# Kernel tuning notes

Measured on AMD Instinct MI355X. Metric: run time of the kernel, lower is better.

The kernel has to match this reference:

```python
import jax, jax.numpy as jnp
from jax import lax
import numpy as np

NUM_CLASSES = 81
SCALES = (64.0, 128.0, 256.0)
RATIOS = (0.5, 1.0, 2.0)
A = 9                       # anchors per cell = len(SCALES)*len(RATIOS)
POOL = 14
PRE_NMS = 6000
PROPOSAL_COUNT = 1000
NMS_THR = 0.7
BN_EPS = 1e-3               # keras BatchNormalization default epsilon
NEG = -1e9                  # suppressed-score sentinel (avoids -inf NaNs in grad)


def conv(x, w, b, padding):
    return lax.conv_general_dilated(x, w, (1, 1), padding,
        dimension_numbers=('NHWC', 'HWIO', 'NHWC')) + b


def bn(x, g, b, m, v):
    # inference-mode batch norm
    return (x - m) * (g / jnp.sqrt(v + BN_EPS)) + b


def generate_anchors(fh, fw, H, W):
    sy, sx = H / fh, W / fw
    scales = jnp.asarray(SCALES, jnp.float32)
    sq = jnp.sqrt(jnp.asarray(RATIOS, jnp.float32))
    ah = (scales[:, None] * sq[None, :]).reshape(-1)   # [A]
    aw = (scales[:, None] / sq[None, :]).reshape(-1)
    cy = (jnp.arange(fh, dtype=jnp.float32) + 0.5) * sy
    cx = (jnp.arange(fw, dtype=jnp.float32) + 0.5) * sx
    cy, cx = jnp.meshgrid(cy, cx, indexing='ij')
    cy, cx = cy[..., None], cx[..., None]              # [fh,fw,1]
    # (y1, x1, y2, x2), flattened per-cell-then-anchor to match channel layout
    return jnp.stack([cy - ah / 2, cx - aw / 2, cy + ah / 2, cx + aw / 2], -1).reshape(-1, 4)


def decode(anchors, deltas):
    h = anchors[:, 2] - anchors[:, 0]
    w = anchors[:, 3] - anchors[:, 1]
    cy = anchors[:, 0] + 0.5 * h + deltas[:, 0] * h
    cx = anchors[:, 1] + 0.5 * w + deltas[:, 1] * w
    h = h * jnp.exp(deltas[:, 2])
    w = w * jnp.exp(deltas[:, 3])
    return jnp.stack([cy - 0.5 * h, cx - 0.5 * w, cy + 0.5 * h, cx + 0.5 * w], 1)


def iou_one_vs_all(box, boxes):
    y1 = jnp.maximum(box[0], boxes[:, 0]); x1 = jnp.maximum(box[1], boxes[:, 1])
    y2 = jnp.minimum(box[2], boxes[:, 2]); x2 = jnp.minimum(box[3], boxes[:, 3])
    inter = jnp.maximum(y2 - y1, 0.0) * jnp.maximum(x2 - x1, 0.0)
    a = (box[2] - box[0]) * (box[3] - box[1])
    b = (boxes[:, 2] - boxes[:, 0]) * (boxes[:, 3] - boxes[:, 1])
    return inter / (a + b - inter + 1e-8)


def nms(boxes, scores, max_out, thr):
    # greedy NMS with fixed iteration count (jit-friendly)
    def step(s, _):
        i = jnp.argmax(s)
        valid = s[i] > NEG * 0.5
        sup = iou_one_vs_all(boxes[i], boxes) > thr
        s = jnp.where(sup, NEG, s).at[i].set(NEG)
        return s, (i, valid)
    _, (idx, valid) = lax.scan(step, scores, None, length=max_out)
    return idx, valid


def roi_align(feat, boxes):
    # feat: [H, W, C]; boxes: [N, 4] normalized (y1, x1, y2, x2)
    H, W, _ = feat.shape
    t = jnp.arange(POOL, dtype=jnp.float32) / (POOL - 1)
    def one(box):
        y1, x1, y2, x2 = box
        ys = (y1 + t * (y2 - y1)) * (H - 1)
        xs = (x1 + t * (x2 - x1)) * (W - 1)
        y0 = jnp.clip(jnp.floor(ys), 0, H - 2).astype(jnp.int32)
        x0 = jnp.clip(jnp.floor(xs), 0, W - 2).astype(jnp.int32)
        wy = jnp.clip(ys - y0, 0.0, 1.0)[:, None, None]
        wx = jnp.clip(xs - x0, 0.0, 1.0)[None, :, None]
        r0, r1 = feat[y0], feat[y0 + 1]                    # [P, W, C]
        top = r0[:, x0] * (1 - wx) + r0[:, x0 + 1] * wx    # [P, P, C]
        bot = r1[:, x0] * (1 - wx) + r1[:, x0 + 1] * wx
        return top * (1 - wy) + bot * wy
    return jax.vmap(one)(boxes)                            # [N, P, P, C]


def setup_inputs() -> dict:
    key = jax.random.key(0)
    ks = jax.random.split(key, 12)
    f = lambda k, shp, s=0.02: jax.random.normal(k, shp, jnp.float32) * s
    C_in, C_fpn, C_rpn = 1024, 256, 512
    return dict(
        feature=jax.random.normal(ks[0], (1, 64, 64, C_in), jnp.float32),
        w_fpn1=f(ks[1], (1, 1, C_in, C_fpn)), b_fpn1=jnp.zeros((C_fpn,), jnp.float32),
        w_fpn2=f(ks[2], (3, 3, C_fpn, C_fpn)), b_fpn2=jnp.zeros((C_fpn,), jnp.float32),
        w_rpn=f(ks[3], (3, 3, C_fpn, C_rpn)), b_rpn=jnp.zeros((C_rpn,), jnp.float32),
        w_cls=f(ks[4], (1, 1, C_rpn, A * 2)), b_cls=jnp.zeros((A * 2,), jnp.float32),
        w_dlt=f(ks[5], (1, 1, C_rpn, A * 4)), b_dlt=jnp.zeros((A * 4,), jnp.float32),
        w_rc1=f(ks[6], (POOL, POOL, C_fpn, 1024), 0.005), b_rc1=jnp.zeros((1024,), jnp.float32),
        g1=jnp.ones((1024,), jnp.float32), be1=jnp.zeros((1024,), jnp.float32),
        m1=jnp.zeros((1024,), jnp.float32), v1=jnp.ones((1024,), jnp.float32),
        w_rc2=f(ks[7], (1024, 1024)), b_rc2=jnp.zeros((1024,), jnp.float32),
        g2=jnp.ones((1024,), jnp.float32), be2=jnp.zeros((1024,), jnp.float32),
        m2=jnp.zeros((1024,), jnp.float32), v2=jnp.ones((1024,), jnp.float32),
        w_log=f(ks[8], (1024, NUM_CLASSES)), b_log=jnp.zeros((NUM_CLASSES,), jnp.float32),
        w_bfc=f(ks[9], (1024, NUM_CLASSES * 4)), b_bfc=jnp.zeros((NUM_CLASSES * 4,), jnp.float32),
        image_h=512, image_w=512,
    )


def reference(feature, w_fpn1, b_fpn1, w_fpn2, b_fpn2, w_rpn, b_rpn, w_cls, b_cls,
              w_dlt, b_dlt, w_rc1, b_rc1, g1, be1, m1, v1, w_rc2, b_rc2, g2, be2,
              m2, v2, w_log, b_log, w_bfc, b_bfc, image_h, image_w):
    H, W = float(image_h), float(image_w)
    # ---- FPN neck: 1x1 then 3x3 conv to 256ch ----
    x = conv(feature, w_fpn1, b_fpn1, 'VALID')
    x = conv(x, w_fpn2, b_fpn2, 'SAME')                # [1, fh, fw, 256]
    fh, fw = x.shape[1], x.shape[2]
    # ---- RPN head ----
    shared = jax.nn.relu(conv(x, w_rpn, b_rpn, 'SAME'))
    rpn_logits = conv(shared, w_cls, b_cls, 'VALID').reshape(-1, 2)
    rpn_probs = jax.nn.softmax(rpn_logits, axis=-1)    # [num_anchors, 2]
    rpn_deltas = conv(shared, w_dlt, b_dlt, 'VALID').reshape(-1, 4)
    # ---- proposal generation: anchors -> top-k -> decode -> clip -> NMS ----
    anchors = generate_anchors(fh, fw, H, W)
    scores = rpn_probs[:, 1]
    k = min(PRE_NMS, anchors.shape[0])
    top_scores, ix = lax.top_k(scores, k)
    props = decode(anchors[ix], rpn_deltas[ix])
    window = jnp.asarray([H, W, H, W], jnp.float32)
    props = jnp.minimum(jnp.maximum(props, 0.0), window)   # bbox_clip
    props = props / window                                  # normalize
    sel, valid = nms(props, top_scores, PROPOSAL_COUNT, NMS_THR)
    proposals = props[sel] * valid[:, None].astype(props.dtype)  # [1000, 4]
    # ---- RoI pooling + RCNN head ----
    rois = roi_align(x[0], proposals)                       # [1000, 14, 14, 256]
    h1 = rois.reshape(PROPOSAL_COUNT, -1) @ w_rc1.reshape(-1, 1024) + b_rc1
    h1 = jax.nn.relu(bn(h1, g1, be1, m1, v1))
    h2 = jax.nn.relu(bn(h1 @ w_rc2 + b_rc2, g2, be2, m2, v2))
    cls_probs = jax.nn.softmax(h2 @ w_log + b_log, axis=-1)         # [1000, 81]
    box_deltas = (h2 @ w_bfc + b_bfc).reshape(-1, NUM_CLASSES, 4)   # [1000, 81, 4]
    return (rpn_probs.reshape(1, -1, 2), rpn_deltas.reshape(1, -1, 4),
            proposals, cls_probs, box_deltas)
```

## Files before the change

kernel.cpp:

```cpp
#include <hip/hip_runtime.h>
#include <hip/hip_bf16.h>

typedef unsigned int u32;
typedef unsigned long long u64;
typedef unsigned short u16;

typedef float f32x4 __attribute__((ext_vector_type(4)));
typedef __bf16 bf16x8 __attribute__((ext_vector_type(8)));
typedef unsigned short u16x8 __attribute__((ext_vector_type(8)));
typedef unsigned short u16x4 __attribute__((ext_vector_type(4)));

#define NA 36864
#define PRE_NMS 6000
#define NPROP 1000
#define KROI 50176
#define SORTN 8192
#define MASKW 94
#define MASKT_STRIDE 6144
#define KSPLIT 8
#define KCHUNK (KROI / KSPLIT)
#define BN_EPS 1e-3f

__device__ __forceinline__ u16 f2bf(float v) {
    __bf16 h = (__bf16)v;
    return __builtin_bit_cast(u16, h);
}
__device__ __forceinline__ bf16x8 ldfrag(const u16* p) {
    return __builtin_bit_cast(bf16x8, *(const u16x8*)p);
}
__device__ __forceinline__ void gload16(const void* g, void* l) {
    __builtin_amdgcn_global_load_lds(
        (const __attribute__((address_space(1))) unsigned int*)g,
        (__attribute__((address_space(3))) unsigned int*)l, 16, 0, 0);
}

template <bool CONV3>
__global__ __launch_bounds__(128) void gemm_v3(
    const float* __restrict__ A, const float* __restrict__ B, float* __restrict__ part,
    int M, int N, int K, int kchunk) {
    __shared__ float As[2][16][132];
    __shared__ float Bs[2][16][68];
    const int tid = threadIdx.x;
    const int bm = blockIdx.x * 128, bn = blockIdx.y * 64;
    const int ks = blockIdx.z;
    const int kbeg = ks * kchunk, kend = kbeg + kchunk;
    const int tx = tid & 7, ty = tid >> 3;
    (void)K;

    float4 ra[4], rb[2];
    auto loadA = [&](int k0, int i) -> float4 {
        int e = tid + 128 * i;
        int m = e >> 2, kq = (e & 3) * 4;
        float4 v = {0.f, 0.f, 0.f, 0.f};
        int gm = bm + m;
        if (CONV3) {
            int gg = k0 >> 8;
            int dy = gg / 3, dx = gg - 3 * dy;
            int pr = gm >> 6, pc = gm & 63;
            int sr = pr + dy - 1, sc = pc + dx - 1;
            int ch = (k0 & 255) + kq;
            if (sr >= 0 && sr < 64 && sc >= 0 && sc < 64)
                v = *(const float4*)&A[(size_t)((sr << 6) + sc) * 256 + ch];
        } else {
            if (gm < M) v = *(const float4*)&A[(size_t)gm * K + k0 + kq];
        }
        return v;
    };
    auto loadB = [&](int k0, int i) -> float4 {
        int e = tid + 128 * i;
        int n4 = (e & 15) * 4, kk = e >> 4;
        return *(const float4*)&B[(size_t)(k0 + kk) * N + bn + n4];
    };
    auto stage = [&](int s) {
#pragma unroll
        for (int i = 0; i < 4; ++i) {
            int e = tid + 128 * i; int m = e >> 2, kq = (e & 3) * 4;
            As[s][kq + 0][m] = ra[i].x; As[s][kq + 1][m] = ra[i].y;
            As[s][kq + 2][m] = ra[i].z; As[s][kq + 3][m] = ra[i].w;
        }
#pragma unroll
        for (int i = 0; i < 2; ++i) {
            int e = tid + 128 * i; int n4 = (e & 15) * 4, kk = e >> 4;
            *(float4*)&Bs[s][kk][n4] = rb[i];
        }
    };

    float acc[8][8] = {};
#pragma unroll
    for (int i = 0; i < 4; ++i) ra[i] = loadA(kbeg, i);
#pragma unroll
    for (int i = 0; i < 2; ++i) rb[i] = loadB(kbeg, i);
    stage(0);
    if (kbeg + 16 < kend) {
#pragma unroll
        for (int i = 0; i < 4; ++i) ra[i] = loadA(kbeg + 16, i);
#pragma unroll
        for (int i = 0; i < 2; ++i) rb[i] = loadB(kbeg + 16, i);
    }
    __syncthreads();
    int s = 0;
    for (int k0 = kbeg; k0 < kend; k0 += 16) {
        if (k0 + 16 < kend) {
            stage(s ^ 1);
            if (k0 + 32 < kend) {
#pragma unroll
                for (int i = 0; i < 4; ++i) ra[i] = loadA(k0 + 32, i);
#pragma unroll
                for (int i = 0; i < 2; ++i) rb[i] = loadB(k0 + 32, i);
            }
        }
#pragma unroll
        for (int kk = 0; kk < 16; ++kk) {
            float4 a0 = *(const float4*)&As[s][kk][8 * ty];
            float4 a1 = *(const float4*)&As[s][kk][8 * ty + 4];
            float4 b0 = *(const float4*)&Bs[s][kk][8 * tx];
            float4 b1 = *(const float4*)&Bs[s][kk][8 * tx + 4];
            const float av[8] = {a0.x, a0.y, a0.z, a0.w, a1.x, a1.y, a1.z, a1.w};
            const float bv[8] = {b0.x, b0.y, b0.z, b0.w, b1.x, b1.y, b1.z, b1.w};
#pragma unroll
            for (int r = 0; r < 8; ++r)
#pragma unroll
                for (int c = 0; c < 8; ++c) acc[r][c] = fmaf(av[r], bv[c], acc[r][c]);
        }
        __syncthreads();
        s ^= 1;
    }
    float* P = part + (size_t)ks * ((size_t)M * N);
#pragma unroll
    for (int r = 0; r < 8; ++r) {
        int gm = bm + 8 * ty + r;
        if (gm >= M) continue;
        *(float4*)&P[(size_t)gm * N + bn + 8 * tx] = *(const float4*)&acc[r][0];
        *(float4*)&P[(size_t)gm * N + bn + 8 * tx + 4] = *(const float4*)&acc[r][4];
    }
}

template <int EPI>
__global__ __launch_bounds__(256) void reduce_part(
    const float* __restrict__ part, float* __restrict__ C, int M, int N, int KS,
    const float* __restrict__ bias, const float* __restrict__ g,
    const float* __restrict__ be, const float* __restrict__ mu,
    const float* __restrict__ var) {
    int i = blockIdx.x * 256 + threadIdx.x;
    int total = (M * N) >> 2;
    if (i >= total) return;
    size_t off = (size_t)i * 4;
    int n = (int)(off % (size_t)N);
    size_t slice = (size_t)M * N;
    float4 sv = {0.f, 0.f, 0.f, 0.f};
    for (int k = 0; k < KS; ++k) {
        float4 v = *(const float4*)&part[(size_t)k * slice + off];
        sv.x += v.x; sv.y += v.y; sv.z += v.z; sv.w += v.w;
    }
    float o[4] = {sv.x, sv.y, sv.z, sv.w};
#pragma unroll
    for (int j = 0; j < 4; ++j) {
        float v = o[j] + bias[n + j];
        if constexpr (EPI == 1) v = fmaxf(v, 0.f);
        if constexpr (EPI == 2) {
            float sc = g[n + j] / sqrtf(var[n + j] + BN_EPS);
            v = (v - mu[n + j]) * sc + be[n + j];
            v = fmaxf(v, 0.f);
        }
        o[j] = v;
    }
    *(float4*)&C[off] = *(const float4*)&o[0];
}

__global__ __launch_bounds__(256) void pack_heads(
    const float* __restrict__ wc, const float* __restrict__ wd,
    const float* __restrict__ bc, const float* __restrict__ bd,
    float* __restrict__ wCat, float* __restrict__ bCat) {
    int i = blockIdx.x * 256 + threadIdx.x;
    if (i < 512 * 64) {
        int k = i >> 6, n = i & 63;
        float v = 0.f;
        if (n < 18) v = wc[k * 18 + n];
        else if (n < 54) v = wd[k * 36 + (n - 18)];
        wCat[i] = v;
    }
    if (i < 64) bCat[i] = (i < 18) ? bc[i] : ((i < 54) ? bd[i - 18] : 0.f);
}

__global__ __launch_bounds__(256) void split_dlt(
    const float* __restrict__ hc, float* __restrict__ out1) {
    int i = blockIdx.x * 256 + threadIdx.x;
    if (i >= 4096 * 36) return;
    int cell = i / 36, r = i - cell * 36;
    out1[i] = hc[cell * 64 + 18 + r];
}

__global__ __launch_bounds__(256) void pack_roi_heads(
    const float* __restrict__ wl, const float* __restrict__ wb,
    const float* __restrict__ bl, const float* __restrict__ bb,
    float* __restrict__ wH, float* __restrict__ bH) {
    int i = blockIdx.x * 256 + threadIdx.x;
    if (i < 1024 * 512) {
        int k = i >> 9, n = i & 511;
        float v = 0.f;
        if (n < 81) v = wl[k * 81 + n];
        else if (n < 405) v = wb[k * 324 + (n - 81)];
        wH[i] = v;
    }
    if (i < 512) bH[i] = (i < 81) ? bl[i] : ((i < 405) ? bb[i - 81] : 0.f);
}

__global__ __launch_bounds__(256) void split_roi(
    const float* __restrict__ hr, float* __restrict__ logitsT, float* __restrict__ out4) {
    int i = blockIdx.x * 256 + threadIdx.x;
    if (i < NPROP * 81) {
        int r = i / 81, c = i - r * 81;
        logitsT[i] = hr[r * 512 + c];
    }
    if (i < NPROP * 324) {
        int r = i / 324, c = i - r * 324;
        out4[i] = hr[r * 512 + 81 + c];
    }
}

__global__ __launch_bounds__(256) void rpn_probs_keys(
    const float* __restrict__ hc, float* __restrict__ out0, u64* __restrict__ keys) {
    int i = blockIdx.x * 256 + threadIdx.x;
    if (i >= NA) return;
    int cell = i / 9, a = i - cell * 9;
    float l0 = hc[cell * 64 + 2 * a], l1 = hc[cell * 64 + 2 * a + 1];
    float m = fmaxf(l0, l1);
    float e0 = expf(l0 - m), e1 = expf(l1 - m);
    float ssum = e0 + e1;
    float p0 = e0 / ssum, p1 = e1 / ssum;
    out0[2 * i] = p0;
    out0[2 * i + 1] = p1;
    keys[i] = ((u64)__float_as_uint(p1) << 32) | (u64)(0xFFFFFFFFu - (u32)i);
}

__global__ __launch_bounds__(1024) void radix_select(
    const u64* __restrict__ keys, u64* __restrict__ thresh, u32* __restrict__ counter) {
    __shared__ u32 hist[256];
    __shared__ u64 sPrefix, sMask;
    __shared__ int sRank;
    int tid = threadIdx.x;
    if (tid == 0) { sPrefix = 0; sMask = 0; sRank = PRE_NMS; }
    __syncthreads();
    for (int p = 56; p >= 0; p -= 8) {
        if (tid < 256) hist[tid] = 0;
        __syncthreads();
        u64 pref = sPrefix, msk = sMask;
        for (int i = tid; i < NA; i += 1024) {
            u64 k = keys[i];
            if ((k & msk) == pref) atomicAdd(&hist[(u32)((k >> p) & 255)], 1u);
        }
        __syncthreads();
        if (tid == 0) {
            int cum = 0, rank = sRank, sel = 0;
            for (int d = 255; d >= 0; --d) {
                int c = (int)hist[d];
                if (cum + c >= rank) { sel = d; sRank = rank - cum; break; }
                cum += c;
            }
            sPrefix = pref | ((u64)(u32)sel << p);
            sMask = msk | (0xFFull << p);
        }
        __syncthreads();
    }
    if (tid == 0) { thresh[0] = sPrefix; *counter = 0; }
}

__global__ __launch_bounds__(256) void compact_topk(
    const u64* __restrict__ keys, const u64* __restrict__ thresh,
    u32* __restrict__ counter, u64* __restrict__ skeys) {
    int i = blockIdx.x * 256 + threadIdx.x;
    if (i < SORTN - PRE_NMS) skeys[PRE_NMS + i] = 0;
    if (i >= NA) return;
    u64 k = keys[i];
    if (k >= thresh[0]) {
        u32 pos = atomicAdd(counter, 1u);
        skeys[pos] = k;
    }
}

__global__ __launch_bounds__(1024) void sort_topk(u64* __restrict__ skeys) {
    __shared__ u64 s[SORTN];
    int tid = threadIdx.x;
    for (int i = tid; i < SORTN; i += 1024) s[i] = skeys[i];
    __syncthreads();
    for (int k = 2; k <= SORTN; k <<= 1) {
        for (int j = k >> 1; j > 0; j >>= 1) {
            for (int i = tid; i < SORTN; i += 1024) {
                int ixj = i ^ j;
                if (ixj > i) {
                    u64 a = s[i], b = s[ixj];
                    bool up = ((i & k) == 0);
                    bool sw = up ? (a < b) : (a > b);
                    if (sw) { s[i] = b; s[ixj] = a; }
                }
            }
            __syncthreads();
        }
    }
    for (int i = tid; i < SORTN; i += 1024) skeys[i] = s[i];
}

__global__ __launch_bounds__(256) void decode_props(
    const u64* __restrict__ skeys, const float* __restrict__ deltas,
    const int* __restrict__ ih, const int* __restrict__ iw, float* __restrict__ props) {
    int i = blockIdx.x * 256 + threadIdx.x;
    if (i >= PRE_NMS) return;
    u32 idx = 0xFFFFFFFFu - (u32)(skeys[i] & 0xFFFFFFFFull);
    float H = (float)(*ih), W = (float)(*iw);
    int a = idx % 9;
    int cell = idx / 9;
    int r = cell >> 6, c = cell & 63;
    float sy = H / 64.0f, sx = W / 64.0f;
    float cy = ((float)r + 0.5f) * sy, cx = ((float)c + 0.5f) * sx;
    const float scales[3] = {64.f, 128.f, 256.f};
    const float ratios[3] = {0.5f, 1.f, 2.f};
    float sq = sqrtf(ratios[a % 3]);
    float scl = scales[a / 3];
    float ah = scl * sq, aw = scl / sq;
    float ay1 = cy - ah * 0.5f, ax1 = cx - aw * 0.5f;
    float h = ah, w = aw;
    float d0 = deltas[(size_t)idx * 4 + 0], d1 = deltas[(size_t)idx * 4 + 1];
    float d2 = deltas[(size_t)idx * 4 + 2], d3 = deltas[(size_t)idx * 4 + 3];
    float ncy = ay1 + 0.5f * h + d0 * h;
    float ncx = ax1 + 0.5f * w + d1 * w;
    float nh = h * expf(d2), nw = w * expf(d3);
    float y1 = ncy - 0.5f * nh, x1 = ncx - 0.5f * nw;
    float y2 = ncy + 0.5f * nh, x2 = ncx + 0.5f * nw;
    props[i * 4 + 0] = fminf(fmaxf(y1, 0.f), H) / H;
    props[i * 4 + 1] = fminf(fmaxf(x1, 0.f), W) / W;
    props[i * 4 + 2] = fminf(fmaxf(y2, 0.f), H) / H;
    props[i * 4 + 3] = fminf(fmaxf(x2, 0.f), W) / W;
}

__global__ __launch_bounds__(256) void nms_masks(
    const float* __restrict__ props, u64* __restrict__ masksT, u64* __restrict__ diag) {
    int i = blockIdx.x * 256 + threadIdx.x;
    int w = blockIdx.y;
    if (i >= PRE_NMS) return;
    float y1 = props[i * 4], x1 = props[i * 4 + 1], y2 = props[i * 4 + 2], x2 = props[i * 4 + 3];
    float ai = (y2 - y1) * (x2 - x1);
    u64 bits = 0;
    int jbase = w * 64;
    for (int b = 0; b < 64; ++b) {
        int j = jbase + b;
        if (j >= PRE_NMS) break;
        float by1 = props[j * 4], bx1 = props[j * 4 + 1], by2 = props[j * 4 + 2], bx2 = props[j * 4 + 3];
        float iy1 = fmaxf(y1, by1), ix1 = fmaxf(x1, bx1);
        float iy2 = fminf(y2, by2), ix2 = fminf(x2, bx2);
        float inter = fmaxf(iy2 - iy1, 0.f) * fmaxf(ix2 - ix1, 0.f);
        float aj = (by2 - by1) * (bx2 - bx1);
        float iou = inter / (ai + aj - inter + 1e-8f);
        if (iou > 0.7f) bits |= (1ull << b);
    }
    masksT[(size_t)w * MASKT_STRIDE + i] = bits;
    if (w == (i >> 6)) diag[i] = bits;
}

__global__ __launch_bounds__(512) void nms_greedy(
    const u64* __restrict__ masksT, const u64* __restrict__ diag,
    int* __restrict__ sel, int* __restrict__ keptOut) {
    __shared__ u64 sdiag[PRE_NMS];
    __shared__ int skept[NPROP];
    __shared__ u64 sword[2];
    __shared__ int skcount;
    const int tid = threadIdx.x;
    const int lane = tid & 63;
    for (int i = tid; i < PRE_NMS; i += 512) sdiag[i] = diag[i];
    if (tid == 0) { sword[0] = 0; sword[1] = 0; skcount = 0; }
    __syncthreads();
    int kept = 0;
    for (int c = 0; c < MASKW; ++c) {
        int keptNow = skcount;
        if (keptNow >= NPROP) break;
        u64 acc = 0;
        const u64* mrow = masksT + (size_t)c * MASKT_STRIDE;
        for (int t = tid; t < keptNow; t += 512) acc |= mrow[skept[t]];
#pragma unroll
        for (int s = 32; s > 0; s >>= 1) acc |= __shfl_xor(acc, s);
        if (lane == 0 && acc) {
            u32* p = (u32*)&sword[c & 1];
            u32 lo = (u32)acc, hi = (u32)(acc >> 32);
            if (lo) atomicOr(&p[0], lo);
            if (hi) atomicOr(&p[1], hi);
        }
        __syncthreads();
        if (tid < 64) {
            int jbase = c * 64;
            u64 removed = sword[c & 1];
            int limit = PRE_NMS - jbase;
            u64 alive = ~removed;
            if (limit < 64) alive &= (1ull << limit) - 1ull;
            u64 mymask = (jbase + lane < PRE_NMS) ? sdiag[jbase + lane] : 0ull;
            while (alive && kept < NPROP) {
                int b = __ffsll((long long)alive) - 1;
                alive &= ~(1ull << b);
                u64 m = __shfl(mymask, b);
                if (lane == 0) {
                    sel[kept] = jbase + b;
                    skept[kept] = jbase + b;
                }
                ++kept;
                alive &= ~m;
            }
            if (lane == 0) skcount = kept;
        } else if (tid == 64) {
            sword[(c + 1) & 1] = 0;
        }
        __syncthreads();
    }
    if (tid == 0) *keptOut = skcount;
}

__global__ __launch_bounds__(256) void write_proposals(
    const float* __restrict__ props, const int* __restrict__ sel,
    const int* __restrict__ keptPtr, float* __restrict__ out2) {
    int i = blockIdx.x * 256 + threadIdx.x;
    if (i >= NPROP * 4) return;
    int p = i >> 2, d = i & 3;
    int kept = *keptPtr;
    out2[i] = (p < kept) ? props[sel[p] * 4 + d] : 0.f;
}

__global__ __launch_bounds__(256) void roi_align_k(
    const float* __restrict__ X2, const float* __restrict__ boxes, u16* __restrict__ rois) {
    int p = blockIdx.x;
    int c = threadIdx.x;
    float y1 = boxes[p * 4], x1 = boxes[p * 4 + 1], y2 = boxes[p * 4 + 2], x2 = boxes[p * 4 + 3];
    for (int py = 0; py < 14; ++py) {
        float ty = (float)py / 13.0f;
        float ys = (y1 + ty * (y2 - y1)) * 63.0f;
        float fy = fminf(fmaxf(floorf(ys), 0.f), 62.f);
        int y0 = (int)fy;
        float wy = fminf(fmaxf(ys - fy, 0.f), 1.f);
        for (int px = 0; px < 14; ++px) {
            float tx = (float)px / 13.0f;
            float xs = (x1 + tx * (x2 - x1)) * 63.0f;
            float fx = fminf(fmaxf(floorf(xs), 0.f), 62.f);
            int x0 = (int)fx;
            float wx = fminf(fmaxf(xs - fx, 0.f), 1.f);
            const float* r0 = X2 + (size_t)((y0) * 64 + x0) * 256 + c;
            const float* r1 = r0 + 64 * 256;
            float v00 = r0[0], v01 = r0[256];
            float v10 = r1[0], v11 = r1[256];
            float top = v00 * (1.f - wx) + v01 * wx;
            float bot = v10 * (1.f - wx) + v11 * wx;
            float v = top * (1.f - wy) + bot * wy;
            rois[((size_t)p * 196 + py * 14 + px) * 256 + c] = f2bf(v);
        }
    }
}

__global__ __launch_bounds__(256) void convert_w1(
    const float* __restrict__ Wf, u16* __restrict__ WT) {
    __shared__ u16 tile[64][72];
    int k0 = blockIdx.x * 64, n0 = blockIdx.y * 64;
    int tid = threadIdx.x;
#pragma unroll
    for (int i = 0; i < 4; ++i) {
        int e = tid + 256 * i;
        int kk = e >> 4, n4 = (e & 15) * 4;
        float4 v = *(const float4*)&Wf[(size_t)(k0 + kk) * 1024 + n0 + n4];
        tile[kk][n4 + 0] = f2bf(v.x);
        tile[kk][n4 + 1] = f2bf(v.y);
        tile[kk][n4 + 2] = f2bf(v.z);
        tile[kk][n4 + 3] = f2bf(v.w);
    }
    __syncthreads();
#pragma unroll
    for (int i = 0; i < 4; ++i) {
        int e = tid + 256 * i;
        int k4 = (e & 15) * 4, nn = e >> 4;
        u16x4 o = {tile[k4 + 0][nn], tile[k4 + 1][nn], tile[k4 + 2][nn], tile[k4 + 3][nn]};
        *(u16x4*)&WT[(size_t)(n0 + nn) * KROI + k0 + k4] = o;
    }
}

__global__ __launch_bounds__(256) void h1_gemm(
    const u16* __restrict__ Abf, const u16* __restrict__ Bbf, float* __restrict__ part) {
    const int tid = threadIdx.x;
    const int bid = blockIdx.x;
    const int ks = bid & 7;
    const int bm = ((bid >> 3) & 7) * 128;
    const int bn = (bid >> 6) * 128;
    __shared__ u16 As[128 * 64];
    __shared__ u16 Bs[128 * 64];
    const int wave = tid >> 6, lane = tid & 63;
    const size_t kbase = (size_t)ks * KCHUNK;
    const int wm = (wave >> 1) * 64, wn = (wave & 1) * 64;
    const int fr = lane & 15, fg = lane >> 4;
    const int srow = wave * 32 + (lane >> 3);
    const int scol = (((lane & 7) ^ (lane >> 3)) * 8);
    const size_t abase = (size_t)(bm + srow) * KROI + kbase + scol;
    const size_t bbase = (size_t)(bn + srow) * KROI + kbase + scol;
    u16* AsW = &As[wave * 2048];
    u16* BsW = &Bs[wave * 2048];

    f32x4 acc[4][4] = {};
    for (int k0 = 0; k0 < KCHUNK; k0 += 64) {
        __syncthreads();
#pragma unroll
        for (int i = 0; i < 4; ++i) {
            gload16(Abf + abase + (size_t)(i * 8) * KROI + k0, AsW + i * 512);
            gload16(Bbf + bbase + (size_t)(i * 8) * KROI + k0, BsW + i * 512);
        }
        __syncthreads();
        bf16x8 fa[4][2], fb[4][2];
#pragma unroll
        for (int t = 0; t < 4; ++t) {
#pragma unroll
            for (int s = 0; s < 2; ++s) {
                int ca = ((s * 4 + fg) ^ (fr & 7)) * 8;
                fa[t][s] = ldfrag(&As[(wm + t * 16 + fr) * 64 + ca]);
                fb[t][s] = ldfrag(&Bs[(wn + t * 16 + fr) * 64 + ca]);
            }
        }
#pragma unroll
        for (int s = 0; s < 2; ++s)
#pragma unroll
            for (int mi = 0; mi < 4; ++mi)
#pragma unroll
                for (int nj = 0; nj < 4; ++nj)
                    acc[mi][nj] = __builtin_amdgcn_mfma_f32_16x16x32_bf16(
                        fa[mi][s], fb[nj][s], acc[mi][nj], 0, 0, 0);
    }
    float* P = part + ((size_t)ks << 20);
#pragma unroll
    for (int mi = 0; mi < 4; ++mi) {
#pragma unroll
        for (int nj = 0; nj < 4; ++nj) {
            int r0 = bm + wm + mi * 16 + fg * 4;
            int c0 = bn + wn + nj * 16 + fr;
#pragma unroll
            for (int j = 0; j < 4; ++j)
                if (r0 + j < NPROP) P[(size_t)(r0 + j) * 1024 + c0] = acc[mi][nj][j];
        }
    }
}

__global__ __launch_bounds__(256) void reduce_h1(
    const float* __restrict__ part, const float* __restrict__ bias,
    const float* __restrict__ g, const float* __restrict__ be,
    const float* __restrict__ mu, const float* __restrict__ var, float* __restrict__ h1) {
    int i = blockIdx.x * 256 + threadIdx.x;
    if (i >= NPROP * 1024) return;
    int n = i & 1023, m = i >> 10;
    float s = 0.f;
#pragma unroll
    for (int k = 0; k < KSPLIT; ++k) s += part[((size_t)k << 20) + ((size_t)m << 10) + n];
    s += bias[n];
    float sc = g[n] / sqrtf(var[n] + BN_EPS);
    s = (s - mu[n]) * sc + be[n];
    h1[i] = fmaxf(s, 0.f);
}

__global__ __launch_bounds__(128) void softmax_cls(
    const float* __restrict__ logits, float* __restrict__ out3) {
    __shared__ float sm[128];
    int row = blockIdx.x, t = threadIdx.x;
    float v = (t < 81) ? logits[(size_t)row * 81 + t] : -1e30f;
    sm[t] = v;
    __syncthreads();
    for (int s = 64; s > 0; s >>= 1) {
        if (t < s) sm[t] = fmaxf(sm[t], sm[t + s]);
        __syncthreads();
    }
    float mx = sm[0];
    __syncthreads();
    float e = (t < 81) ? expf(v - mx) : 0.f;
    sm[t] = e;
    __syncthreads();
    for (int s = 64; s > 0; s >>= 1) {
        if (t < s) sm[t] += sm[t + s];
        __syncthreads();
    }
    float denom = sm[0];
    if (t < 81) out3[(size_t)row * 81 + t] = e / denom;
}

extern "C" void kernel_launch(void* const* d_in, const int* in_sizes, int n_in,
                              void* d_out, int out_size, void* d_ws, size_t ws_size,
                              hipStream_t stream) {
    const float* feature = (const float*)d_in[0];
    const float* w_fpn1 = (const float*)d_in[1];
    const float* b_fpn1 = (const float*)d_in[2];
    const float* w_fpn2 = (const float*)d_in[3];
    const float* b_fpn2 = (const float*)d_in[4];
    const float* w_rpn = (const float*)d_in[5];
    const float* b_rpn = (const float*)d_in[6];
    const float* w_cls = (const float*)d_in[7];
    const float* b_cls = (const float*)d_in[8];
    const float* w_dlt = (const float*)d_in[9];
    const float* b_dlt = (const float*)d_in[10];
    const float* w_rc1 = (const float*)d_in[11];
    const float* b_rc1 = (const float*)d_in[12];
    const float* g1 = (const float*)d_in[13];
    const float* be1 = (const float*)d_in[14];
    const float* m1 = (const float*)d_in[15];
    const float* v1 = (const float*)d_in[16];
    const float* w_rc2 = (const float*)d_in[17];
    const float* b_rc2 = (const float*)d_in[18];
    const float* g2 = (const float*)d_in[19];
    const float* be2 = (const float*)d_in[20];
    const float* m2 = (const float*)d_in[21];
    const float* v2 = (const float*)d_in[22];
    const float* w_log = (const float*)d_in[23];
    const float* b_log = (const float*)d_in[24];
    const float* w_bfc = (const float*)d_in[25];
    const float* b_bfc = (const float*)d_in[26];
    const int* image_h = (const int*)d_in[27];
    const int* image_w = (const int*)d_in[28];
    (void)in_sizes; (void)n_in; (void)out_size; (void)ws_size;

    float* out0 = (float*)d_out;
    float* out1 = out0 + 73728;
    float* out2 = out1 + 147456;
    float* out3 = out2 + 4000;
    float* out4 = out3 + 81000;

    char* wsb = (char*)d_ws;
    size_t off = 0;
    auto take = [&](size_t b) -> void* {
        off = (off + 255) & ~(size_t)255;
        void* p = wsb + off;
        off += b;
        return p;
    };
    float* x1 = (float*)take((size_t)4096 * 256 * 4);
    float* x2 = (float*)take((size_t)4096 * 256 * 4);
    float* shr = (float*)take((size_t)4096 * 512 * 4);
    float* hcat = (float*)take((size_t)4096 * 64 * 4);
    float* wCat = (float*)take((size_t)512 * 64 * 4);
    float* bCat = (float*)take((size_t)64 * 4);
    float* wHead = (float*)take((size_t)1024 * 512 * 4);
    float* bHead = (float*)take((size_t)512 * 4);
    float* hroi = (float*)take((size_t)NPROP * 512 * 4);
    u64* keys = (u64*)take((size_t)NA * 8);
    u64* skeys = (u64*)take((size_t)SORTN * 8);
    float* props = (float*)take((size_t)PRE_NMS * 4 * 4);
    u64* masksT = (u64*)take((size_t)MASKW * MASKT_STRIDE * 8);
    u64* diag = (u64*)take((size_t)PRE_NMS * 8);
    int* sel = (int*)take((size_t)NPROP * 4);
    u64* misc = (u64*)take(256);
    u32* counter = (u32*)((char*)misc + 8);
    int* keptp = (int*)((char*)misc + 16);
    u16* rois = (u16*)take((size_t)NPROP * KROI * 2);
    u16* wT = (u16*)take((size_t)1024 * KROI * 2);
    float* part = (float*)take((size_t)KSPLIT * 1024 * 1024 * 4);
    float* h1 = (float*)take((size_t)NPROP * 1024 * 4);
    float* h2 = (float*)take((size_t)NPROP * 1024 * 4);
    float* logitsT = (float*)take((size_t)NPROP * 81 * 4);

    gemm_v3<false><<<dim3(32, 4, 8), 128, 0, stream>>>(feature, w_fpn1, part, 4096, 256, 1024, 128);
    reduce_part<0><<<dim3(1024), 256, 0, stream>>>(part, x1, 4096, 256, 8, b_fpn1, nullptr, nullptr, nullptr, nullptr);
    gemm_v3<true><<<dim3(32, 4, 8), 128, 0, stream>>>(x1, w_fpn2, part, 4096, 256, 2304, 288);
    reduce_part<0><<<dim3(1024), 256, 0, stream>>>(part, x2, 4096, 256, 8, b_fpn2, nullptr, nullptr, nullptr, nullptr);
    gemm_v3<true><<<dim3(32, 8, 4), 128, 0, stream>>>(x2, w_rpn, part, 4096, 512, 2304, 576);
    reduce_part<1><<<dim3(2048), 256, 0, stream>>>(part, shr, 4096, 512, 4, b_rpn, nullptr, nullptr, nullptr, nullptr);
    pack_heads<<<dim3(128), 256, 0, stream>>>(w_cls, w_dlt, b_cls, b_dlt, wCat, bCat);
    gemm_v3<false><<<dim3(32, 1, 8), 128, 0, stream>>>(shr, wCat, part, 4096, 64, 512, 64);
    reduce_part<0><<<dim3(256), 256, 0, stream>>>(part, hcat, 4096, 64, 8, bCat, nullptr, nullptr, nullptr, nullptr);
    split_dlt<<<dim3(576), 256, 0, stream>>>(hcat, out1);
    rpn_probs_keys<<<dim3(144), 256, 0, stream>>>(hcat, out0, keys);

    radix_select<<<1, 1024, 0, stream>>>(keys, misc, counter);
    compact_topk<<<dim3(144), 256, 0, stream>>>(keys, misc, counter, skeys);
    sort_topk<<<1, 1024, 0, stream>>>(skeys);
    decode_props<<<dim3(24), 256, 0, stream>>>(skeys, out1, image_h, image_w, props);
    nms_masks<<<dim3(24, 94), 256, 0, stream>>>(props, masksT, diag);
    nms_greedy<<<1, 512, 0, stream>>>(masksT, diag, sel, keptp);
    write_proposals<<<dim3(16), 256, 0, stream>>>(props, sel, keptp, out2);

    convert_w1<<<dim3(784, 16), 256, 0, stream>>>(w_rc1, wT);
    roi_align_k<<<dim3(1000), 256, 0, stream>>>(x2, out2, rois);
    h1_gemm<<<dim3(512), 256, 0, stream>>>(rois, wT, part);
    reduce_h1<<<dim3(4000), 256, 0, stream>>>(part, b_rc1, g1, be1, m1, v1, h1);
    gemm_v3<false><<<dim3(8, 16, 2), 128, 0, stream>>>(h1, w_rc2, part, 1000, 1024, 1024, 512);
    reduce_part<2><<<dim3(1000), 256, 0, stream>>>(part, h2, 1000, 1024, 2, b_rc2, g2, be2, m2, v2);
    pack_roi_heads<<<dim3(2048), 256, 0, stream>>>(w_log, w_bfc, b_log, b_bfc, wHead, bHead);
    gemm_v3<false><<<dim3(8, 8, 2), 128, 0, stream>>>(h2, wHead, part, 1000, 512, 1024, 512);
    reduce_part<0><<<dim3(500), 256, 0, stream>>>(part, hroi, 1000, 512, 2, bHead, nullptr, nullptr, nullptr, nullptr);
    split_roi<<<dim3(1266), 256, 0, stream>>>(hroi, logitsT, out4);
    softmax_cls<<<dim3(1000), 128, 0, stream>>>(logitsT, out3);
}
```

Measured before the change: 1.116 ms.

## Replace bitonic top-k sort with rank sort; overlap weight conversion with greedy NMS

The single-block bitonic sort over 8192 padded keys is replaced by a 24-block rank sort, where each thread counts how many of the 6000 keys are larger and scatters its key to that position. This assumes the keys are unique, which holds because each key embeds the anchor index. The w_rc1 fp32-to-bf16 transpose kernel is folded into the serial single-block greedy NMS launch as extra blocks, so the weight conversion can use idle CUs while block 0 runs NMS. The risk is that conversion blocks launched ahead of or alongside block 0 could delay it, and each rank-sort thread does O(N) shared-memory reads.

```diff
diff --git a/kernel.cpp b/kernel.cpp
--- a/kernel.cpp
+++ b/kernel.cpp
@@ -14,12 +14,12 @@
 #define PRE_NMS 6000
 #define NPROP 1000
 #define KROI 50176
-#define SORTN 8192
 #define MASKW 94
 #define MASKT_STRIDE 6144
 #define KSPLIT 8
 #define KCHUNK (KROI / KSPLIT)
 #define BN_EPS 1e-3f
+#define CONV_TILES 12544
 
 __device__ __forceinline__ u16 f2bf(float v) {
     __bf16 h = (__bf16)v;
@@ -269,7 +269,6 @@
     const u64* __restrict__ keys, const u64* __restrict__ thresh,
     u32* __restrict__ counter, u64* __restrict__ skeys) {
     int i = blockIdx.x * 256 + threadIdx.x;
-    if (i < SORTN - PRE_NMS) skeys[PRE_NMS + i] = 0;
     if (i >= NA) return;
     u64 k = keys[i];
     if (k >= thresh[0]) {
@@ -278,26 +277,19 @@
     }
 }
 
-__global__ __launch_bounds__(1024) void sort_topk(u64* __restrict__ skeys) {
-    __shared__ u64 s[SORTN];
-    int tid = threadIdx.x;
-    for (int i = tid; i < SORTN; i += 1024) s[i] = skeys[i];
+__global__ __launch_bounds__(256) void rank_sort(
+    const u64* __restrict__ skeys, u64* __restrict__ sorted) {
+    __shared__ u64 lds[PRE_NMS];
+    const int tid = threadIdx.x;
+    for (int i = tid; i < PRE_NMS; i += 256) lds[i] = skeys[i];
     __syncthreads();
-    for (int k = 2; k <= SORTN; k <<= 1) {
-        for (int j = k >> 1; j > 0; j >>= 1) {
-            for (int i = tid; i < SORTN; i += 1024) {
-                int ixj = i ^ j;
-                if (ixj > i) {
-                    u64 a = s[i], b = s[ixj];
-                    bool up = ((i & k) == 0);
-                    bool sw = up ? (a < b) : (a > b);
-                    if (sw) { s[i] = b; s[ixj] = a; }
-                }
-            }
-            __syncthreads();
-        }
-    }
-    for (int i = tid; i < SORTN; i += 1024) skeys[i] = s[i];
+    int i = blockIdx.x * 256 + tid;
+    if (i >= PRE_NMS) return;
+    u64 k = lds[i];
+    int c = 0;
+#pragma unroll 4
+    for (int j = 0; j < PRE_NMS; ++j) c += (lds[j] > k) ? 1 : 0;
+    sorted[c] = k;
 }
 
 __global__ __launch_bounds__(256) void decode_props(
@@ -356,14 +348,41 @@
     if (w == (i >> 6)) diag[i] = bits;
 }
 
-__global__ __launch_bounds__(512) void nms_greedy(
+__global__ __launch_bounds__(512) void nms_greedy_conv(
     const u64* __restrict__ masksT, const u64* __restrict__ diag,
-    int* __restrict__ sel, int* __restrict__ keptOut) {
+    int* __restrict__ sel, int* __restrict__ keptOut,
+    const float* __restrict__ Wf, u16* __restrict__ WT) {
     __shared__ u64 sdiag[PRE_NMS];
     __shared__ int skept[NPROP];
     __shared__ u64 sword[2];
     __shared__ int skcount;
     const int tid = threadIdx.x;
+
+    if (blockIdx.x != 0) {
+        u16 (*tile)[72] = (u16(*)[72])sdiag;
+        int bid = blockIdx.x - 1;
+        int k0 = (bid % 784) * 64, n0 = (bid / 784) * 64;
+#pragma unroll
+        for (int i = 0; i < 2; ++i) {
+            int e = tid + 512 * i;
+            int kk = e >> 4, n4 = (e & 15) * 4;
+            float4 v = *(const float4*)&Wf[(size_t)(k0 + kk) * 1024 + n0 + n4];
+            tile[kk][n4 + 0] = f2bf(v.x);
+            tile[kk][n4 + 1] = f2bf(v.y);
+            tile[kk][n4 + 2] = f2bf(v.z);
+            tile[kk][n4 + 3] = f2bf(v.w);
+        }
+        __syncthreads();
+#pragma unroll
+        for (int i = 0; i < 2; ++i) {
+            int e = tid + 512 * i;
+            int k4 = (e & 15) * 4, nn = e >> 4;
+            u16x4 o = {tile[k4 + 0][nn], tile[k4 + 1][nn], tile[k4 + 2][nn], tile[k4 + 3][nn]};
+            *(u16x4*)&WT[(size_t)(n0 + nn) * KROI + k0 + k4] = o;
+        }
+        return;
+    }
+
     const int lane = tid & 63;
     for (int i = tid; i < PRE_NMS; i += 512) sdiag[i] = diag[i];
     if (tid == 0) { sword[0] = 0; sword[1] = 0; skcount = 0; }
@@ -447,31 +466,6 @@
             float v = top * (1.f - wy) + bot * wy;
             rois[((size_t)p * 196 + py * 14 + px) * 256 + c] = f2bf(v);
         }
-    }
-}
-
-__global__ __launch_bounds__(256) void convert_w1(
-    const float* __restrict__ Wf, u16* __restrict__ WT) {
-    __shared__ u16 tile[64][72];
-    int k0 = blockIdx.x * 64, n0 = blockIdx.y * 64;
-    int tid = threadIdx.x;
-#pragma unroll
-    for (int i = 0; i < 4; ++i) {
-        int e = tid + 256 * i;
-        int kk = e >> 4, n4 = (e & 15) * 4;
-        float4 v = *(const float4*)&Wf[(size_t)(k0 + kk) * 1024 + n0 + n4];
-        tile[kk][n4 + 0] = f2bf(v.x);
-        tile[kk][n4 + 1] = f2bf(v.y);
-        tile[kk][n4 + 2] = f2bf(v.z);
-        tile[kk][n4 + 3] = f2bf(v.w);
-    }
-    __syncthreads();
-#pragma unroll
-    for (int i = 0; i < 4; ++i) {
-        int e = tid + 256 * i;
-        int k4 = (e & 15) * 4, nn = e >> 4;
-        u16x4 o = {tile[k4 + 0][nn], tile[k4 + 1][nn], tile[k4 + 2][nn], tile[k4 + 3][nn]};
-        *(u16x4*)&WT[(size_t)(n0 + nn) * KROI + k0 + k4] = o;
     }
 }
 
@@ -635,7 +629,8 @@
     float* bHead = (float*)take((size_t)512 * 4);
     float* hroi = (float*)take((size_t)NPROP * 512 * 4);
     u64* keys = (u64*)take((size_t)NA * 8);
-    u64* skeys = (u64*)take((size_t)SORTN * 8);
+    u64* skeys = (u64*)take((size_t)PRE_NMS * 8);
+    u64* sortedK = (u64*)take((size_t)PRE_NMS * 8);
     float* props = (float*)take((size_t)PRE_NMS * 4 * 4);
     u64* masksT = (u64*)take((size_t)MASKW * MASKT_STRIDE * 8);
     u64* diag = (u64*)take((size_t)PRE_NMS * 8);
@@ -664,13 +659,12 @@
 
     radix_select<<<1, 1024, 0, stream>>>(keys, misc, counter);
     compact_topk<<<dim3(144), 256, 0, stream>>>(keys, misc, counter, skeys);
-    sort_topk<<<1, 1024, 0, stream>>>(skeys);
-    decode_props<<<dim3(24), 256, 0, stream>>>(skeys, out1, image_h, image_w, props);
+    rank_sort<<<dim3(24), 256, 0, stream>>>(skeys, sortedK);
+    decode_props<<<dim3(24), 256, 0, stream>>>(sortedK, out1, image_h, image_w, props);
     nms_masks<<<dim3(24, 94), 256, 0, stream>>>(props, masksT, diag);
-    nms_greedy<<<1, 512, 0, stream>>>(masksT, diag, sel, keptp);
+    nms_greedy_conv<<<dim3(1 + CONV_TILES), 512, 0, stream>>>(masksT, diag, sel, keptp, w_rc1, wT);
     write_proposals<<<dim3(16), 256, 0, stream>>>(props, sel, keptp, out2);
 
-    convert_w1<<<dim3(784, 16), 256, 0, stream>>>(w_rc1, wT);
     roi_align_k<<<dim3(1000), 256, 0, stream>>>(x2, out2, rois);
     h1_gemm<<<dim3(512), 256, 0, stream>>>(rois, wT, part);
     reduce_h1<<<dim3(4000), 256, 0, stream>>>(part, b_rc1, g1, be1, m1, v1, h1);
```

After: 1.068 ms. -4.3%, faster.
